# Kernel tuning notes

Hardware: AMD Instinct MI355X
Metric: run time of the kernel (lower is better)

Reference implementation:

```python
import math
import jax, jax.numpy as jnp
import numpy as np

NUM_EXPERTS = 8
CAPACITY_FACTOR = 1.5

def setup_inputs() -> dict:
    key = jax.random.key(0)
    ks = jax.random.split(key, 4)
    B, T, D, F, E = 4, 2048, 1024, 4096, NUM_EXPERTS
    scale = 0.02
    return {
        "x": jax.random.normal(ks[0], (B, T, D), dtype=jnp.float32),
        "router_w": jax.random.normal(ks[1], (E, D), dtype=jnp.float32) * scale,  # nn.Linear(D,E,bias=False).weight
        "w1": jax.random.normal(ks[2], (E, D, F), dtype=jnp.float32) * scale,
        "b1": jnp.zeros((E, F), dtype=jnp.float32),
        "w2": jax.random.normal(ks[3], (E, F, D), dtype=jnp.float32) * scale,
        "b2": jnp.zeros((E, D), dtype=jnp.float32),
    }

def reference(x, router_w, w1, b1, w2, b2):
    B, T, D = x.shape
    E = router_w.shape[0]
    N = B * T
    C = max(math.ceil(CAPACITY_FACTOR * N / E), 1)  # static per-expert capacity

    x_flat = x.reshape(N, D)
    logits = x_flat @ router_w.T                      # [N, E]
    probs = jax.nn.softmax(logits, axis=-1)
    chosen_e = jnp.argmax(probs, axis=-1)             # [N] int
    chosen_p = jnp.max(probs, axis=-1)                # [N]

    # First-come-first-served capacity: position of each token within its expert's queue
    onehot = jax.nn.one_hot(chosen_e, E, dtype=jnp.float32)          # [N, E]
    pos = jnp.take_along_axis(jnp.cumsum(onehot, axis=0), chosen_e[:, None], axis=1)[:, 0] - 1.0
    pos = pos.astype(jnp.int32)                                       # [N]
    kept = (pos < C)                                                  # [N] bool
    pos_c = jnp.clip(pos, 0, C - 1)

    # Scatter tokens into per-expert capacity buffers [E, C, D]; dropped tokens contribute 0
    buf = jnp.zeros((E, C, D), dtype=x.dtype).at[chosen_e, pos_c].add(
        x_flat * kept[:, None].astype(x.dtype))

    # Expert FFN: Linear -> exact GELU -> Linear (torch nn.GELU default = erf)
    h = jax.nn.gelu(jnp.einsum('ecd,edf->ecf', buf, w1) + b1[:, None, :], approximate=False)
    eo = jnp.einsum('ecf,efd->ecd', h, w2) + b2[:, None, :]           # [E, C, D]

    # Gather back and scale by router prob; dropped tokens get zeros
    y = eo[chosen_e, pos_c] * (chosen_p * kept.astype(x.dtype))[:, None]
    return y.reshape(B, T, D)
```

## Files before the change

kernel.cpp:

```cpp
#include <hip/hip_runtime.h>
#include <hip/hip_bf16.h>
#include <math.h>

typedef unsigned short u16;
typedef __attribute__((ext_vector_type(8))) short short8;
typedef __attribute__((ext_vector_type(4))) float f32x4;

#define NTOK 8192
#define DMODEL 1024
#define FDIM 4096
#define NEXP 8
#define CAP 1536

__device__ __forceinline__ u16 f2bf(float f) {
  __hip_bfloat16 b = __float2bfloat16(f);
  u16 u;
  __builtin_memcpy(&u, &b, 2);
  return u;
}

__device__ __forceinline__ float gelu_exact(float v) {
  float x = v * 0.70710678118654752f;
  float ax = fabsf(x);
  float t = __builtin_amdgcn_rcpf(1.0f + 0.3275911f * ax);
  float p =
      t * (0.254829592f +
           t * (-0.284496736f +
                t * (1.421413741f + t * (-1.453152027f + t * 1.061405429f))));
  float er = 1.0f - p * __expf(-ax * ax);
  er = copysignf(er, x);
  return 0.5f * v * (1.0f + er);
}

__device__ __forceinline__ void gload_lds16(const u16* g, u16* l) {
  __builtin_amdgcn_global_load_lds(
      (const __attribute__((address_space(1))) void*)g,
      (__attribute__((address_space(3))) void*)l, 16, 0, 0);
}

__global__ __launch_bounds__(256) void router_kernel(
    const float* __restrict__ x, const float* __restrict__ rw,
    int* __restrict__ chosen_e, float* __restrict__ chosen_p) {
  int b = blockIdx.x, tid = threadIdx.x;
  int tok = (b * 256 + tid) >> 6;
  int lane = tid & 63;
  const float4* xp = (const float4*)(x + (size_t)tok * DMODEL) + lane * 4;
  float4 x0 = xp[0], x1 = xp[1], x2 = xp[2], x3 = xp[3];
  float l[8];
#pragma unroll
  for (int e = 0; e < 8; e++) {
    const float4* wp = (const float4*)(rw + (size_t)e * DMODEL) + lane * 4;
    float4 w0 = wp[0], w1v = wp[1], w2v = wp[2], w3 = wp[3];
    float s = x0.x * w0.x + x0.y * w0.y + x0.z * w0.z + x0.w * w0.w;
    s += x1.x * w1v.x + x1.y * w1v.y + x1.z * w1v.z + x1.w * w1v.w;
    s += x2.x * w2v.x + x2.y * w2v.y + x2.z * w2v.z + x2.w * w2v.w;
    s += x3.x * w3.x + x3.y * w3.y + x3.z * w3.z + x3.w * w3.w;
    l[e] = s;
  }
#pragma unroll
  for (int off = 32; off > 0; off >>= 1) {
#pragma unroll
    for (int e = 0; e < 8; e++) l[e] += __shfl_xor(l[e], off, 64);
  }
  if (lane == 0) {
    float best = l[0];
    int am = 0;
#pragma unroll
    for (int e = 1; e < 8; e++)
      if (l[e] > best) { best = l[e]; am = e; }
    float denom = 0.f;
#pragma unroll
    for (int e = 0; e < 8; e++) denom += expf(l[e] - best);
    chosen_e[tok] = am;
    chosen_p[tok] = 1.0f / denom;
  }
}

__device__ __forceinline__ void trans256(const float* __restrict__ ip,
                                         u16* __restrict__ op, int Rin,
                                         int Cin, int r0, int c0, char* lds,
                                         int tid) {
  int w = tid >> 6, l = tid & 63;
#pragma unroll
  for (int i = 0; i < 16; i++) {
    int row = w * 16 + i;
    float4 v = *(const float4*)(ip + (size_t)(r0 + row) * Cin + c0 + l * 4);
    uint2 d;
    d.x = (unsigned)f2bf(v.x) | ((unsigned)f2bf(v.y) << 16);
    d.y = (unsigned)f2bf(v.z) | ((unsigned)f2bf(v.w) << 16);
    int ch = (l >> 1) ^ ((row >> 3) & 7);
    *(uint2*)(lds + row * 512 + ch * 16 + (l & 1) * 8) = d;
  }
  __syncthreads();
#pragma unroll
  for (int p = 0; p < 2; p++) {
    int c = ((tid >> 5) + p * 32) * 4;
    int rb = (tid & 31) * 8;
    short8 s0, s1, s2, s3;
#pragma unroll
    for (int j = 0; j < 8; j++) {
      int r = rb + j;
      int ch = (c >> 3) ^ ((r >> 3) & 7);
      uint2 d = *(const uint2*)(lds + r * 512 + ch * 16 + (c & 7) * 2);
      s0[j] = (short)(d.x & 0xffff);
      s1[j] = (short)(d.x >> 16);
      s2[j] = (short)(d.y & 0xffff);
      s3[j] = (short)(d.y >> 16);
    }
    u16* ob = op + (size_t)((r0 + rb) >> 5) * Cin * 32 +
              (size_t)(c0 + c) * 32 + ((r0 + rb) & 31);
    *(short8*)(ob) = s0;
    *(short8*)(ob + 32) = s1;
    *(short8*)(ob + 64) = s2;
    *(short8*)(ob + 96) = s3;
  }
}

__global__ __launch_bounds__(1024, 1) void wtrans_kernel(
    const float* __restrict__ w1, const float* __restrict__ w2,
    u16* __restrict__ w1t, u16* __restrict__ w2t,
    const int* __restrict__ chosen_e, int* __restrict__ tok_of_slot,
    int* __restrict__ counts, float* __restrict__ out) {
  extern __shared__ char lds[];
  int b = blockIdx.x, tid = threadIdx.x;
  if (b == 0) {
    if (tid < 512) {
      int w = tid >> 6, lane = tid & 63;
      unsigned long long ltmask =
          (lane == 63) ? ~0ull >> 1 : (1ull << lane) - 1ull;
      int cnt = 0;
      for (int c = 0; c < NTOK / 64; c++) {
        int i = c * 64 + lane;
        int e = chosen_e[i];
        unsigned long long bal = __ballot(e == w);
        if (e == w) {
          int p = cnt + __popcll(bal & ltmask);
          if (p < CAP) {
            tok_of_slot[w * CAP + p] = i;
          } else {
            float4 z = make_float4(0.f, 0.f, 0.f, 0.f);
            float* orow = out + (size_t)i * DMODEL;
            for (int d = 0; d < DMODEL; d += 4) *(float4*)(orow + d) = z;
          }
        }
        cnt += __popcll(bal);
      }
      for (int p = cnt + lane; p < CAP; p += 64) tok_of_slot[w * CAP + p] = -1;
      if (lane == 0) counts[w] = cnt < CAP ? cnt : CAP;
    }
  } else if (b < 513) {
    int idx = b - 1;
    int e = idx >> 6, rem = idx & 63;
    int r0 = (rem >> 4) * 256, c0 = (rem & 15) * 256;
    trans256(w1 + (size_t)e * DMODEL * FDIM, w1t + (size_t)e * DMODEL * FDIM,
             DMODEL, FDIM, r0, c0, lds, tid);
  } else {
    int idx = b - 513;
    int e = idx >> 6, rem = idx & 63;
    int r0 = (rem >> 2) * 256, c0 = (rem & 3) * 256;
    trans256(w2 + (size_t)e * DMODEL * FDIM, w2t + (size_t)e * DMODEL * FDIM,
             FDIM, DMODEL, r0, c0, lds, tid);
  }
}

__global__ __launch_bounds__(256) void gather_kernel(
    const float* __restrict__ x, const int* __restrict__ tok_of_slot,
    u16* __restrict__ xg) {
  int slot = blockIdx.x * 4 + (threadIdx.x >> 6);
  int lane = threadIdx.x & 63;
  int tok = tok_of_slot[slot];
  u16* dst = xg + (size_t)slot * DMODEL + lane * 16;
  if (tok < 0) {
    short8 z = {};
    *(short8*)(dst) = z;
    *(short8*)(dst + 8) = z;
    return;
  }
  const float4* sp = (const float4*)(x + (size_t)tok * DMODEL) + lane * 4;
  float4 a = sp[0], b = sp[1], c = sp[2], d = sp[3];
  short8 s0, s1;
  s0[0] = (short)f2bf(a.x); s0[1] = (short)f2bf(a.y);
  s0[2] = (short)f2bf(a.z); s0[3] = (short)f2bf(a.w);
  s0[4] = (short)f2bf(b.x); s0[5] = (short)f2bf(b.y);
  s0[6] = (short)f2bf(b.z); s0[7] = (short)f2bf(b.w);
  s1[0] = (short)f2bf(c.x); s1[1] = (short)f2bf(c.y);
  s1[2] = (short)f2bf(c.z); s1[3] = (short)f2bf(c.w);
  s1[4] = (short)f2bf(d.x); s1[5] = (short)f2bf(d.y);
  s1[6] = (short)f2bf(d.z); s1[7] = (short)f2bf(d.w);
  *(short8*)(dst) = s0;
  *(short8*)(dst + 8) = s1;
}

template <int NX, int NY>
__device__ __forceinline__ void tile_coords(int& bx, int& by, int& bz) {
  int flat = blockIdx.x + NX * (blockIdx.y + NY * blockIdx.z);
  int nwg = NX * NY * (int)gridDim.z;
  int swz = (flat & 7) * (nwg >> 3) + (flat >> 3);
  bx = swz % NX;
  int rem = swz / NX;
  by = rem % NY;
  bz = rem / NY;
}

template <int KD>
__device__ __forceinline__ void mainloop_db(const u16* pa0, const u16* pa1,
                                            const u16* pb0, const u16* pb1,
                                            size_t bstep, u16* smem,
                                            f32x4 (&acc)[4][4], int tid) {
  int wid = tid >> 6, lane = tid & 63;
  int wm = (wid >> 1) * 64, wn = (wid & 1) * 64;
  int fr = lane & 15, fk = (lane >> 4) * 8;
  int aro = (wm + fr) * 32 + fk;
  int bro = 4096 + (wn + fr) * 32 + fk;
  gload_lds16(pa0, smem + tid * 8);
  gload_lds16(pa1, smem + 2048 + tid * 8);
  gload_lds16(pb0, smem + 4096 + tid * 8);
  gload_lds16(pb1, smem + 6144 + tid * 8);
  __syncthreads();
  int cur = 0;
#pragma unroll 1
  for (int t = 0; t < KD / 32; ++t) {
    const u16* cb = smem + cur * 8192;
    u16* nb = smem + (cur ^ 1) * 8192;
    if (t + 1 < KD / 32) {
      gload_lds16(pa0 + (t + 1) * 32, nb + tid * 8);
      gload_lds16(pa1 + (t + 1) * 32, nb + 2048 + tid * 8);
      gload_lds16(pb0 + (size_t)(t + 1) * bstep, nb + 4096 + tid * 8);
      gload_lds16(pb1 + (size_t)(t + 1) * bstep, nb + 6144 + tid * 8);
    }
    short8 av[4], bv[4];
#pragma unroll
    for (int m = 0; m < 4; m++) av[m] = *(const short8*)(cb + aro + m * 512);
#pragma unroll
    for (int n = 0; n < 4; n++) bv[n] = *(const short8*)(cb + bro + n * 512);
#pragma unroll
    for (int m = 0; m < 4; m++)
#pragma unroll
      for (int n = 0; n < 4; n++)
        acc[m][n] = __builtin_amdgcn_mfma_f32_16x16x32_bf16(av[m], bv[n],
                                                            acc[m][n], 0, 0, 0);
    __syncthreads();
    cur ^= 1;
  }
}

#define VMWAIT(N) asm volatile("s_waitcnt vmcnt(" #N ")" ::: "memory")
#define LGKM0 asm volatile("s_waitcnt lgkmcnt(0)" ::: "memory")

#define G1_STAGE_A(t)                                              \
  {                                                                \
    u16* d_ = smem + ((t) & 3) * 16384 + tid * 8;                  \
    gload_lds16(pa0 + (t) * 32, d_);                               \
    gload_lds16(pa1 + (t) * 32, d_ + 4096);                        \
  }
#define G1_STAGE_B(t)                                              \
  {                                                                \
    u16* d_ = smem + ((t) & 3) * 16384 + 8192 + tid * 8;           \
    gload_lds16(pb0 + (size_t)(t) * (FDIM * 32), d_);              \
    gload_lds16(pb1 + (size_t)(t) * (FDIM * 32), d_ + 4096);       \
  }

#define G1_TILE(t, VMSTMT, DO_ISSUE)                                          \
  {                                                                           \
    const u16* Ab_ = smem + ((t) & 3) * 16384;                                \
    short8 a_[8], b0_, b1_;                                                   \
    _Pragma("unroll") for (int m_ = 0; m_ < 8; m_++) a_[m_] =                 \
        *(const short8*)(Ab_ + aoff + m_ * 512);                              \
    b0_ = *(const short8*)(Ab_ + boff);                                       \
    b1_ = *(const short8*)(Ab_ + boff + 512);                                 \
    if (DO_ISSUE) G1_STAGE_A((t) + 3);                                        \
    __builtin_amdgcn_s_barrier();                                             \
    LGKM0;                                                                    \
    __builtin_amdgcn_s_setprio(1);                                            \
    _Pragma("unroll") for (int m_ = 0; m_ < 8; m_++) {                        \
      acc[m_][0] = __builtin_amdgcn_mfma_f32_16x16x32_bf16(a_[m_], b0_,       \
                                                           acc[m_][0], 0, 0,  \
                                                           0);                \
      acc[m_][1] = __builtin_amdgcn_mfma_f32_16x16x32_bf16(a_[m_], b1_,       \
                                                           acc[m_][1], 0, 0,  \
                                                           0);                \
    }                                                                         \
    __builtin_amdgcn_s_setprio(0);                                            \
    __builtin_amdgcn_s_barrier();                                             \
    short8 b2_ = *(const short8*)(Ab_ + boff + 1024);                         \
    short8 b3_ = *(const short8*)(Ab_ + boff + 1536);                         \
    if (DO_ISSUE) G1_STAGE_B((t) + 3);                                        \
    VMSTMT;                                                                   \
    __builtin_amdgcn_s_barrier();                                             \
    LGKM0;                                                                    \
    __builtin_amdgcn_s_setprio(1);                                            \
    _Pragma("unroll") for (int m_ = 0; m_ < 8; m_++) {                        \
      acc[m_][2] = __builtin_amdgcn_mfma_f32_16x16x32_bf16(a_[m_], b2_,       \
                                                           acc[m_][2], 0, 0,  \
                                                           0);                \
      acc[m_][3] = __builtin_amdgcn_mfma_f32_16x16x32_bf16(a_[m_], b3_,       \
                                                           acc[m_][3], 0, 0,  \
                                                           0);                \
    }                                                                         \
    __builtin_amdgcn_s_setprio(0);                                            \
    __builtin_amdgcn_s_barrier();                                             \
  }

template <int NX, int NY>
__global__ __launch_bounds__(512, 2) void gemm1_kernel(
    const u16* __restrict__ xg, const u16* __restrict__ w1tB,
    const int* __restrict__ counts, u16* __restrict__ hB,
    const float* __restrict__ b1, int e0, long long hStrideE) {
  extern __shared__ __align__(16) u16 smem[];
  int bx, by, bz;
  tile_coords<NX, NY>(bx, by, bz);
  int e = e0 + bz;
  int m0 = by * 256, n0 = bx * 256;
  if (m0 >= counts[e]) return;
  const u16* Bg = w1tB + (size_t)e * FDIM * DMODEL;
  u16* H = hB + (size_t)bz * hStrideE;
  int tid = threadIdx.x;

  int r4 = tid >> 2, c8 = (tid & 3) * 8;
  const u16* pa0 = xg + (size_t)(e * CAP + m0 + r4) * DMODEL + c8;
  const u16* pa1 = pa0 + (size_t)128 * DMODEL;
  const u16* pb0 = Bg + (size_t)(n0 + r4) * 32 + c8;
  const u16* pb1 = pb0 + 128 * 32;

  int wid = tid >> 6, lane = tid & 63;
  int wm = (wid >> 2) * 128, wn = (wid & 3) * 64;
  int fr = lane & 15, fk = (lane >> 4) * 8;
  int aoff = (wm + fr) * 32 + fk;
  int boff = 8192 + (wn + fr) * 32 + fk;
  f32x4 acc[8][4] = {};

  G1_STAGE_A(0); G1_STAGE_B(0);
  G1_STAGE_A(1); G1_STAGE_B(1);
  G1_STAGE_A(2); G1_STAGE_B(2);
  VMWAIT(8);
  __builtin_amdgcn_s_barrier();

  const int KT = DMODEL / 32;
#pragma unroll 1
  for (int t = 0; t < KT - 3; ++t) G1_TILE(t, VMWAIT(8), true);
  G1_TILE(KT - 3, VMWAIT(4), false);
  G1_TILE(KT - 2, VMWAIT(0), false);
  G1_TILE(KT - 1, (void)0, false);

  int fq = lane >> 4;
  const float* b1g = b1 + (size_t)e * FDIM + n0;
  float bias[4];
#pragma unroll
  for (int n = 0; n < 4; n++) bias[n] = b1g[wn + n * 16 + fr];
#pragma unroll
  for (int m = 0; m < 8; m++) {
#pragma unroll
    for (int n = 0; n < 4; n++) {
      int colL = wn + n * 16 + fr;
#pragma unroll
      for (int j = 0; j < 4; j++) {
        int rL = wm + m * 16 + fq * 4 + j;
        float v = gelu_exact(acc[m][n][j] + bias[n]);
        int ch = (colL >> 3) ^ ((rL >> 2) & 7);
        smem[rL * 256 + ch * 8 + (colL & 7)] = f2bf(v);
      }
    }
  }
  __syncthreads();
#pragma unroll
  for (int p = 0; p < 16; p++) {
    int idx = p * 512 + tid;
    int rr = idx >> 5, cch = idx & 31;
    int ch = cch ^ ((rr >> 2) & 7);
    short8 v = *(const short8*)(smem + rr * 256 + ch * 8);
    *(short8*)(H + (size_t)(m0 + rr) * FDIM + n0 + cch * 8) = v;
  }
}

template <int NX, int NY>
__global__ __launch_bounds__(256) void gemm2_kernel(
    const u16* __restrict__ hB, const u16* __restrict__ w2tB,
    float* __restrict__ out, const float* __restrict__ b2,
    const int* __restrict__ tok_of_slot, const int* __restrict__ counts,
    const float* __restrict__ chosen_p, int e0, long long hStrideE) {
  __shared__ __align__(16) u16 smem[16384];
  int bx, by, bz;
  tile_coords<NX, NY>(bx, by, bz);
  int e = e0 + bz;
  int m0 = by * 128, n0 = bx * 128;
  if (m0 >= counts[e]) return;
  const u16* Ag = hB + (size_t)bz * hStrideE;
  const u16* Bg = w2tB + (size_t)e * DMODEL * FDIM;
  const float* b2g = b2 + (size_t)e * DMODEL;
  int tid = threadIdx.x;
  int r2 = tid >> 2, c8 = (tid & 3) * 8;
  const u16* pa0 = Ag + (size_t)(m0 + r2) * FDIM + c8;
  const u16* pa1 = pa0 + (size_t)64 * FDIM;
  const u16* pb0 = Bg + (size_t)(n0 + r2) * 32 + c8;
  const u16* pb1 = pb0 + 64 * 32;
  f32x4 acc[4][4] = {};
  mainloop_db<FDIM>(pa0, pa1, pb0, pb1, (size_t)DMODEL * 32, smem, acc, tid);

  int wid = tid >> 6, lane = tid & 63;
  int wm = (wid >> 1) * 64, wn = (wid & 1) * 64;
  int fr = lane & 15, fq = lane >> 4;
  float bias[4];
#pragma unroll
  for (int n = 0; n < 4; n++) bias[n] = b2g[n0 + wn + n * 16 + fr];
#pragma unroll
  for (int m = 0; m < 4; m++) {
#pragma unroll
    for (int j = 0; j < 4; j++) {
      int rL = wm + m * 16 + fq * 4 + j;
      int tk = tok_of_slot[e * CAP + m0 + rL];
      if (tk >= 0) {
        float sc = chosen_p[tk];
#pragma unroll
        for (int n = 0; n < 4; n++) {
          int colL = wn + n * 16 + fr;
          out[(size_t)tk * DMODEL + n0 + colL] = (acc[m][n][j] + bias[n]) * sc;
        }
      }
    }
  }
}

extern "C" void kernel_launch(void* const* d_in, const int* in_sizes, int n_in,
                              void* d_out, int out_size, void* d_ws,
                              size_t ws_size, hipStream_t stream) {
  const float* x = (const float*)d_in[0];
  const float* rw = (const float*)d_in[1];
  const float* w1 = (const float*)d_in[2];
  const float* b1 = (const float*)d_in[3];
  const float* w2 = (const float*)d_in[4];
  const float* b2 = (const float*)d_in[5];
  float* out = (float*)d_out;

  char* ws = (char*)d_ws;
  size_t off = 0;
  auto alloc = [&](size_t bytes) -> void* {
    void* p = ws + off;
    off = (off + bytes + 255) & ~(size_t)255;
    return p;
  };
  int* chosen_e = (int*)alloc((size_t)NTOK * 4);
  float* chosen_p = (float*)alloc((size_t)NTOK * 4);
  int* tok_of_slot = (int*)alloc((size_t)NEXP * CAP * 4);
  int* counts = (int*)alloc(NEXP * 4);
  u16* xg = (u16*)alloc((size_t)NEXP * CAP * DMODEL * 2);
  u16* w1t = (u16*)alloc((size_t)NEXP * DMODEL * FDIM * 2);
  u16* w2t = (u16*)alloc((size_t)NEXP * DMODEL * FDIM * 2);
  size_t hFull = (size_t)NEXP * CAP * FDIM * 2;
  size_t hLoop = (size_t)CAP * FDIM * 2;
  bool full = (off + hFull) <= ws_size;
  u16* h = (u16*)alloc(full ? hFull : hLoop);

  static_assert(CAP % 256 == 0 && FDIM % 256 == 0 && DMODEL % 128 == 0, "");
  const int TLDS = 131072, G1LDS = 131072;
  hipFuncSetAttribute((const void*)wtrans_kernel,
                      hipFuncAttributeMaxDynamicSharedMemorySize, TLDS);
  hipFuncSetAttribute((const void*)gemm1_kernel<FDIM / 256, CAP / 256>,
                      hipFuncAttributeMaxDynamicSharedMemorySize, G1LDS);

  router_kernel<<<NTOK / 4, 256, 0, stream>>>(x, rw, chosen_e, chosen_p);
  wtrans_kernel<<<1025, 1024, TLDS, stream>>>(w1, w2, w1t, w2t, chosen_e,
                                              tok_of_slot, counts, out);
  gather_kernel<<<NEXP * CAP / 4, 256, 0, stream>>>(x, tok_of_slot, xg);

  if (full) {
    gemm1_kernel<FDIM / 256, CAP / 256>
        <<<dim3(FDIM / 256, CAP / 256, NEXP), 512, G1LDS, stream>>>(
            xg, w1t, counts, h, b1, 0, (long long)CAP * FDIM);
    gemm2_kernel<DMODEL / 128, CAP / 128>
        <<<dim3(DMODEL / 128, CAP / 128, NEXP), 256, 0, stream>>>(
            h, w2t, out, b2, tok_of_slot, counts, chosen_p, 0,
            (long long)CAP * FDIM);
  } else {
    for (int e = 0; e < NEXP; e++) {
      gemm1_kernel<FDIM / 256, CAP / 256>
          <<<dim3(FDIM / 256, CAP / 256, 1), 512, G1LDS, stream>>>(
              xg, w1t, counts, h, b1, e, 0);
      gemm2_kernel<DMODEL / 128, CAP / 128>
          <<<dim3(DMODEL / 128, CAP / 128, 1), 256, 0, stream>>>(
              h, w2t, out, b2, tok_of_slot, counts, chosen_p, e, 0);
    }
  }
  (void)in_sizes;
  (void)n_in;
  (void)ws_size;
}
```

Before: 354.6 us.

## Load B operands directly into registers and stage only A through LDS

```diff
diff --git a/kernel.cpp b/kernel.cpp
--- a/kernel.cpp
+++ b/kernel.cpp
@@ -202,105 +202,6 @@
   bz = rem / NY;
 }
 
-template <int KD>
-__device__ __forceinline__ void mainloop_db(const u16* pa0, const u16* pa1,
-                                            const u16* pb0, const u16* pb1,
-                                            size_t bstep, u16* smem,
-                                            f32x4 (&acc)[4][4], int tid) {
-  int wid = tid >> 6, lane = tid & 63;
-  int wm = (wid >> 1) * 64, wn = (wid & 1) * 64;
-  int fr = lane & 15, fk = (lane >> 4) * 8;
-  int aro = (wm + fr) * 32 + fk;
-  int bro = 4096 + (wn + fr) * 32 + fk;
-  gload_lds16(pa0, smem + tid * 8);
-  gload_lds16(pa1, smem + 2048 + tid * 8);
-  gload_lds16(pb0, smem + 4096 + tid * 8);
-  gload_lds16(pb1, smem + 6144 + tid * 8);
-  __syncthreads();
-  int cur = 0;
-#pragma unroll 1
-  for (int t = 0; t < KD / 32; ++t) {
-    const u16* cb = smem + cur * 8192;
-    u16* nb = smem + (cur ^ 1) * 8192;
-    if (t + 1 < KD / 32) {
-      gload_lds16(pa0 + (t + 1) * 32, nb + tid * 8);
-      gload_lds16(pa1 + (t + 1) * 32, nb + 2048 + tid * 8);
-      gload_lds16(pb0 + (size_t)(t + 1) * bstep, nb + 4096 + tid * 8);
-      gload_lds16(pb1 + (size_t)(t + 1) * bstep, nb + 6144 + tid * 8);
-    }
-    short8 av[4], bv[4];
-#pragma unroll
-    for (int m = 0; m < 4; m++) av[m] = *(const short8*)(cb + aro + m * 512);
-#pragma unroll
-    for (int n = 0; n < 4; n++) bv[n] = *(const short8*)(cb + bro + n * 512);
-#pragma unroll
-    for (int m = 0; m < 4; m++)
-#pragma unroll
-      for (int n = 0; n < 4; n++)
-        acc[m][n] = __builtin_amdgcn_mfma_f32_16x16x32_bf16(av[m], bv[n],
-                                                            acc[m][n], 0, 0, 0);
-    __syncthreads();
-    cur ^= 1;
-  }
-}
-
-#define VMWAIT(N) asm volatile("s_waitcnt vmcnt(" #N ")" ::: "memory")
-#define LGKM0 asm volatile("s_waitcnt lgkmcnt(0)" ::: "memory")
-
-#define G1_STAGE_A(t)                                              \
-  {                                                                \
-    u16* d_ = smem + ((t) & 3) * 16384 + tid * 8;                  \
-    gload_lds16(pa0 + (t) * 32, d_);                               \
-    gload_lds16(pa1 + (t) * 32, d_ + 4096);                        \
-  }
-#define G1_STAGE_B(t)                                              \
-  {                                                                \
-    u16* d_ = smem + ((t) & 3) * 16384 + 8192 + tid * 8;           \
-    gload_lds16(pb0 + (size_t)(t) * (FDIM * 32), d_);              \
-    gload_lds16(pb1 + (size_t)(t) * (FDIM * 32), d_ + 4096);       \
-  }
-
-#define G1_TILE(t, VMSTMT, DO_ISSUE)                                          \
-  {                                                                           \
-    const u16* Ab_ = smem + ((t) & 3) * 16384;                                \
-    short8 a_[8], b0_, b1_;                                                   \
-    _Pragma("unroll") for (int m_ = 0; m_ < 8; m_++) a_[m_] =                 \
-        *(const short8*)(Ab_ + aoff + m_ * 512);                              \
-    b0_ = *(const short8*)(Ab_ + boff);                                       \
-    b1_ = *(const short8*)(Ab_ + boff + 512);                                 \
-    if (DO_ISSUE) G1_STAGE_A((t) + 3);                                        \
-    __builtin_amdgcn_s_barrier();                                             \
-    LGKM0;                                                                    \
-    __builtin_amdgcn_s_setprio(1);                                            \
-    _Pragma("unroll") for (int m_ = 0; m_ < 8; m_++) {                        \
-      acc[m_][0] = __builtin_amdgcn_mfma_f32_16x16x32_bf16(a_[m_], b0_,       \
-                                                           acc[m_][0], 0, 0,  \
-                                                           0);                \
-      acc[m_][1] = __builtin_amdgcn_mfma_f32_16x16x32_bf16(a_[m_], b1_,       \
-                                                           acc[m_][1], 0, 0,  \
-                                                           0);                \
-    }                                                                         \
-    __builtin_amdgcn_s_setprio(0);                                            \
-    __builtin_amdgcn_s_barrier();                                             \
-    short8 b2_ = *(const short8*)(Ab_ + boff + 1024);                         \
-    short8 b3_ = *(const short8*)(Ab_ + boff + 1536);                         \
-    if (DO_ISSUE) G1_STAGE_B((t) + 3);                                        \
-    VMSTMT;                                                                   \
-    __builtin_amdgcn_s_barrier();                                             \
-    LGKM0;                                                                    \
-    __builtin_amdgcn_s_setprio(1);                                            \
-    _Pragma("unroll") for (int m_ = 0; m_ < 8; m_++) {                        \
-      acc[m_][2] = __builtin_amdgcn_mfma_f32_16x16x32_bf16(a_[m_], b2_,       \
-                                                           acc[m_][2], 0, 0,  \
-                                                           0);                \
-      acc[m_][3] = __builtin_amdgcn_mfma_f32_16x16x32_bf16(a_[m_], b3_,       \
-                                                           acc[m_][3], 0, 0,  \
-                                                           0);                \
-    }                                                                         \
-    __builtin_amdgcn_s_setprio(0);                                            \
-    __builtin_amdgcn_s_barrier();                                             \
-  }
-
 template <int NX, int NY>
 __global__ __launch_bounds__(512, 2) void gemm1_kernel(
     const u16* __restrict__ xg, const u16* __restrict__ w1tB,
@@ -319,66 +220,102 @@
   int r4 = tid >> 2, c8 = (tid & 3) * 8;
   const u16* pa0 = xg + (size_t)(e * CAP + m0 + r4) * DMODEL + c8;
   const u16* pa1 = pa0 + (size_t)128 * DMODEL;
-  const u16* pb0 = Bg + (size_t)(n0 + r4) * 32 + c8;
-  const u16* pb1 = pb0 + 128 * 32;
 
   int wid = tid >> 6, lane = tid & 63;
-  int wm = (wid >> 2) * 128, wn = (wid & 3) * 64;
-  int fr = lane & 15, fk = (lane >> 4) * 8;
-  int aoff = (wm + fr) * 32 + fk;
-  int boff = 8192 + (wn + fr) * 32 + fk;
-  f32x4 acc[8][4] = {};
-
-  G1_STAGE_A(0); G1_STAGE_B(0);
-  G1_STAGE_A(1); G1_STAGE_B(1);
-  G1_STAGE_A(2); G1_STAGE_B(2);
-  VMWAIT(8);
-  __builtin_amdgcn_s_barrier();
-
-  const int KT = DMODEL / 32;
+  int wm = (wid >> 1) * 64, wn = (wid & 1) * 128;
+  int fr = lane & 15, fkb = (lane >> 4) * 8;
+  int aoff = (wm + fr) * 32 + fkb;
+  const u16* Bcol = Bg + (size_t)(n0 + wn + fr) * 32 + fkb;
+
+  f32x4 acc[4][8] = {};
+  short8 bA[8], bB[8];
+
+  auto stageA = [&](int t, int buf) {
+    u16* d = smem + buf * 8192 + tid * 8;
+    gload_lds16(pa0 + t * 32, d);
+    gload_lds16(pa1 + t * 32, d + 4096);
+  };
+  auto loadB = [&](short8(&bd)[8], int t) {
+    const u16* p = Bcol + (size_t)t * (FDIM * 32);
+#pragma unroll
+    for (int n = 0; n < 8; n++) bd[n] = *(const short8*)(p + n * 512);
+  };
+  auto compute = [&](int buf, short8(&bd)[8]) {
+    const u16* cb = smem + buf * 8192;
+    short8 av[4];
+#pragma unroll
+    for (int m = 0; m < 4; m++) av[m] = *(const short8*)(cb + aoff + m * 512);
+#pragma unroll
+    for (int m = 0; m < 4; m++)
+#pragma unroll
+      for (int n = 0; n < 8; n++)
+        acc[m][n] = __builtin_amdgcn_mfma_f32_16x16x32_bf16(av[m], bd[n],
+                                                            acc[m][n], 0, 0, 0);
+  };
+
+  stageA(0, 0);
+  loadB(bA, 0);
+  __syncthreads();
 #pragma unroll 1
-  for (int t = 0; t < KT - 3; ++t) G1_TILE(t, VMWAIT(8), true);
-  G1_TILE(KT - 3, VMWAIT(4), false);
-  G1_TILE(KT - 2, VMWAIT(0), false);
-  G1_TILE(KT - 1, (void)0, false);
+  for (int t = 0; t < DMODEL / 32; t += 2) {
+    if (t + 1 < DMODEL / 32) {
+      stageA(t + 1, 1);
+      loadB(bB, t + 1);
+    }
+    compute(0, bA);
+    __syncthreads();
+    if (t + 2 < DMODEL / 32) {
+      stageA(t + 2, 0);
+      loadB(bA, t + 2);
+    }
+    compute(1, bB);
+    __syncthreads();
+  }
 
   int fq = lane >> 4;
   const float* b1g = b1 + (size_t)e * FDIM + n0;
-  float bias[4];
-#pragma unroll
-  for (int n = 0; n < 4; n++) bias[n] = b1g[wn + n * 16 + fr];
-#pragma unroll
-  for (int m = 0; m < 8; m++) {
-#pragma unroll
-    for (int n = 0; n < 4; n++) {
-      int colL = wn + n * 16 + fr;
-#pragma unroll
-      for (int j = 0; j < 4; j++) {
-        int rL = wm + m * 16 + fq * 4 + j;
-        float v = gelu_exact(acc[m][n][j] + bias[n]);
-        int ch = (colL >> 3) ^ ((rL >> 2) & 7);
-        smem[rL * 256 + ch * 8 + (colL & 7)] = f2bf(v);
+  float bias[8];
+#pragma unroll
+  for (int n = 0; n < 8; n++) bias[n] = b1g[wn + n * 16 + fr];
+#pragma unroll
+  for (int half = 0; half < 2; half++) {
+    if ((wid >> 2) == half) {
+      int rbase = wm & 127;
+#pragma unroll
+      for (int m = 0; m < 4; m++) {
+#pragma unroll
+        for (int n = 0; n < 8; n++) {
+          int colL = wn + n * 16 + fr;
+#pragma unroll
+          for (int j = 0; j < 4; j++) {
+            int rL = rbase + m * 16 + fq * 4 + j;
+            float v = gelu_exact(acc[m][n][j] + bias[n]);
+            int ch = (colL >> 3) ^ ((rL >> 2) & 7);
+            smem[rL * 256 + ch * 8 + (colL & 7)] = f2bf(v);
+          }
+        }
       }
     }
-  }
-  __syncthreads();
-#pragma unroll
-  for (int p = 0; p < 16; p++) {
-    int idx = p * 512 + tid;
-    int rr = idx >> 5, cch = idx & 31;
-    int ch = cch ^ ((rr >> 2) & 7);
-    short8 v = *(const short8*)(smem + rr * 256 + ch * 8);
-    *(short8*)(H + (size_t)(m0 + rr) * FDIM + n0 + cch * 8) = v;
+    __syncthreads();
+#pragma unroll
+    for (int p = 0; p < 8; p++) {
+      int idx = p * 512 + tid;
+      int rr = idx >> 5, cch = idx & 31;
+      int ch = cch ^ ((rr >> 2) & 7);
+      short8 v = *(const short8*)(smem + rr * 256 + ch * 8);
+      *(short8*)(H + (size_t)(m0 + half * 128 + rr) * FDIM + n0 + cch * 8) = v;
+    }
+    __syncthreads();
   }
 }
 
 template <int NX, int NY>
-__global__ __launch_bounds__(256) void gemm2_kernel(
+__global__ __launch_bounds__(256, 2) void gemm2_kernel(
     const u16* __restrict__ hB, const u16* __restrict__ w2tB,
     float* __restrict__ out, const float* __restrict__ b2,
     const int* __restrict__ tok_of_slot, const int* __restrict__ counts,
     const float* __restrict__ chosen_p, int e0, long long hStrideE) {
-  __shared__ __align__(16) u16 smem[16384];
+  __shared__ __align__(16) u16 smem[8192];
   int bx, by, bz;
   tile_coords<NX, NY>(bx, by, bz);
   int e = e0 + bz;
@@ -388,17 +325,63 @@
   const u16* Bg = w2tB + (size_t)e * DMODEL * FDIM;
   const float* b2g = b2 + (size_t)e * DMODEL;
   int tid = threadIdx.x;
-  int r2 = tid >> 2, c8 = (tid & 3) * 8;
-  const u16* pa0 = Ag + (size_t)(m0 + r2) * FDIM + c8;
+
+  int r4 = tid >> 2, c8 = (tid & 3) * 8;
+  const u16* pa0 = Ag + (size_t)(m0 + r4) * FDIM + c8;
   const u16* pa1 = pa0 + (size_t)64 * FDIM;
-  const u16* pb0 = Bg + (size_t)(n0 + r2) * 32 + c8;
-  const u16* pb1 = pb0 + 64 * 32;
-  f32x4 acc[4][4] = {};
-  mainloop_db<FDIM>(pa0, pa1, pb0, pb1, (size_t)DMODEL * 32, smem, acc, tid);
 
   int wid = tid >> 6, lane = tid & 63;
   int wm = (wid >> 1) * 64, wn = (wid & 1) * 64;
-  int fr = lane & 15, fq = lane >> 4;
+  int fr = lane & 15, fkb = (lane >> 4) * 8;
+  int aoff = (wm + fr) * 32 + fkb;
+  const u16* Bcol = Bg + (size_t)(n0 + wn + fr) * 32 + fkb;
+
+  f32x4 acc[4][4] = {};
+  short8 bA[4], bB[4];
+
+  auto stageA = [&](int t, int buf) {
+    u16* d = smem + buf * 4096 + tid * 8;
+    gload_lds16(pa0 + t * 32, d);
+    gload_lds16(pa1 + t * 32, d + 2048);
+  };
+  auto loadB = [&](short8(&bd)[4], int t) {
+    const u16* p = Bcol + (size_t)t * (DMODEL * 32);
+#pragma unroll
+    for (int n = 0; n < 4; n++) bd[n] = *(const short8*)(p + n * 512);
+  };
+  auto compute = [&](int buf, short8(&bd)[4]) {
+    const u16* cb = smem + buf * 4096;
+    short8 av[4];
+#pragma unroll
+    for (int m = 0; m < 4; m++) av[m] = *(const short8*)(cb + aoff + m * 512);
+#pragma unroll
+    for (int m = 0; m < 4; m++)
+#pragma unroll
+      for (int n = 0; n < 4; n++)
+        acc[m][n] = __builtin_amdgcn_mfma_f32_16x16x32_bf16(av[m], bd[n],
+                                                            acc[m][n], 0, 0, 0);
+  };
+
+  stageA(0, 0);
+  loadB(bA, 0);
+  __syncthreads();
+#pragma unroll 1
+  for (int t = 0; t < FDIM / 32; t += 2) {
+    if (t + 1 < FDIM / 32) {
+      stageA(t + 1, 1);
+      loadB(bB, t + 1);
+    }
+    compute(0, bA);
+    __syncthreads();
+    if (t + 2 < FDIM / 32) {
+      stageA(t + 2, 0);
+      loadB(bA, t + 2);
+    }
+    compute(1, bB);
+    __syncthreads();
+  }
+
+  int fq = lane >> 4;
   float bias[4];
 #pragma unroll
   for (int n = 0; n < 4; n++) bias[n] = b2g[n0 + wn + n * 16 + fr];
@@ -451,7 +434,7 @@
   u16* h = (u16*)alloc(full ? hFull : hLoop);
 
   static_assert(CAP % 256 == 0 && FDIM % 256 == 0 && DMODEL % 128 == 0, "");
-  const int TLDS = 131072, G1LDS = 131072;
+  const int TLDS = 131072, G1LDS = 65536;
   hipFuncSetAttribute((const void*)wtrans_kernel,
                       hipFuncAttributeMaxDynamicSharedMemorySize, TLDS);
   hipFuncSetAttribute((const void*)gemm1_kernel<FDIM / 256, CAP / 256>,
```

Measured after the change: 429.2 us. 1.21x slower.

## Restructure both expert GEMM mainloops to double-buffered 64-wide K steps

Applied to the files above, without the earlier changes.

```diff
diff --git a/kernel.cpp b/kernel.cpp
--- a/kernel.cpp
+++ b/kernel.cpp
@@ -37,6 +37,11 @@
       (const __attribute__((address_space(1))) void*)g,
       (__attribute__((address_space(3))) void*)l, 16, 0, 0);
 }
+
+#define VMWAIT(N) asm volatile("s_waitcnt vmcnt(" #N ")" ::: "memory")
+#define LGKM0 asm volatile("s_waitcnt lgkmcnt(0)" ::: "memory")
+#define SB0 __builtin_amdgcn_sched_barrier(0)
+#define BAR __builtin_amdgcn_s_barrier()
 
 __global__ __launch_bounds__(256) void router_kernel(
     const float* __restrict__ x, const float* __restrict__ rw,
@@ -202,103 +207,61 @@
   bz = rem / NY;
 }
 
-template <int KD>
-__device__ __forceinline__ void mainloop_db(const u16* pa0, const u16* pa1,
-                                            const u16* pb0, const u16* pb1,
-                                            size_t bstep, u16* smem,
-                                            f32x4 (&acc)[4][4], int tid) {
-  int wid = tid >> 6, lane = tid & 63;
-  int wm = (wid >> 1) * 64, wn = (wid & 1) * 64;
-  int fr = lane & 15, fk = (lane >> 4) * 8;
-  int aro = (wm + fr) * 32 + fk;
-  int bro = 4096 + (wn + fr) * 32 + fk;
-  gload_lds16(pa0, smem + tid * 8);
-  gload_lds16(pa1, smem + 2048 + tid * 8);
-  gload_lds16(pb0, smem + 4096 + tid * 8);
-  gload_lds16(pb1, smem + 6144 + tid * 8);
-  __syncthreads();
-  int cur = 0;
-#pragma unroll 1
-  for (int t = 0; t < KD / 32; ++t) {
-    const u16* cb = smem + cur * 8192;
-    u16* nb = smem + (cur ^ 1) * 8192;
-    if (t + 1 < KD / 32) {
-      gload_lds16(pa0 + (t + 1) * 32, nb + tid * 8);
-      gload_lds16(pa1 + (t + 1) * 32, nb + 2048 + tid * 8);
-      gload_lds16(pb0 + (size_t)(t + 1) * bstep, nb + 4096 + tid * 8);
-      gload_lds16(pb1 + (size_t)(t + 1) * bstep, nb + 6144 + tid * 8);
-    }
-    short8 av[4], bv[4];
-#pragma unroll
-    for (int m = 0; m < 4; m++) av[m] = *(const short8*)(cb + aro + m * 512);
-#pragma unroll
-    for (int n = 0; n < 4; n++) bv[n] = *(const short8*)(cb + bro + n * 512);
-#pragma unroll
-    for (int m = 0; m < 4; m++)
-#pragma unroll
-      for (int n = 0; n < 4; n++)
-        acc[m][n] = __builtin_amdgcn_mfma_f32_16x16x32_bf16(av[m], bv[n],
-                                                            acc[m][n], 0, 0, 0);
-    __syncthreads();
-    cur ^= 1;
-  }
-}
-
-#define VMWAIT(N) asm volatile("s_waitcnt vmcnt(" #N ")" ::: "memory")
-#define LGKM0 asm volatile("s_waitcnt lgkmcnt(0)" ::: "memory")
-
-#define G1_STAGE_A(t)                                              \
-  {                                                                \
-    u16* d_ = smem + ((t) & 3) * 16384 + tid * 8;                  \
-    gload_lds16(pa0 + (t) * 32, d_);                               \
-    gload_lds16(pa1 + (t) * 32, d_ + 4096);                        \
-  }
-#define G1_STAGE_B(t)                                              \
-  {                                                                \
-    u16* d_ = smem + ((t) & 3) * 16384 + 8192 + tid * 8;           \
-    gload_lds16(pb0 + (size_t)(t) * (FDIM * 32), d_);              \
-    gload_lds16(pb1 + (size_t)(t) * (FDIM * 32), d_ + 4096);       \
-  }
-
-#define G1_TILE(t, VMSTMT, DO_ISSUE)                                          \
-  {                                                                           \
-    const u16* Ab_ = smem + ((t) & 3) * 16384;                                \
-    short8 a_[8], b0_, b1_;                                                   \
-    _Pragma("unroll") for (int m_ = 0; m_ < 8; m_++) a_[m_] =                 \
-        *(const short8*)(Ab_ + aoff + m_ * 512);                              \
-    b0_ = *(const short8*)(Ab_ + boff);                                       \
-    b1_ = *(const short8*)(Ab_ + boff + 512);                                 \
-    if (DO_ISSUE) G1_STAGE_A((t) + 3);                                        \
-    __builtin_amdgcn_s_barrier();                                             \
-    LGKM0;                                                                    \
-    __builtin_amdgcn_s_setprio(1);                                            \
-    _Pragma("unroll") for (int m_ = 0; m_ < 8; m_++) {                        \
-      acc[m_][0] = __builtin_amdgcn_mfma_f32_16x16x32_bf16(a_[m_], b0_,       \
-                                                           acc[m_][0], 0, 0,  \
-                                                           0);                \
-      acc[m_][1] = __builtin_amdgcn_mfma_f32_16x16x32_bf16(a_[m_], b1_,       \
-                                                           acc[m_][1], 0, 0,  \
-                                                           0);                \
-    }                                                                         \
-    __builtin_amdgcn_s_setprio(0);                                            \
-    __builtin_amdgcn_s_barrier();                                             \
-    short8 b2_ = *(const short8*)(Ab_ + boff + 1024);                         \
-    short8 b3_ = *(const short8*)(Ab_ + boff + 1536);                         \
-    if (DO_ISSUE) G1_STAGE_B((t) + 3);                                        \
-    VMSTMT;                                                                   \
-    __builtin_amdgcn_s_barrier();                                             \
-    LGKM0;                                                                    \
-    __builtin_amdgcn_s_setprio(1);                                            \
-    _Pragma("unroll") for (int m_ = 0; m_ < 8; m_++) {                        \
-      acc[m_][2] = __builtin_amdgcn_mfma_f32_16x16x32_bf16(a_[m_], b2_,       \
-                                                           acc[m_][2], 0, 0,  \
-                                                           0);                \
-      acc[m_][3] = __builtin_amdgcn_mfma_f32_16x16x32_bf16(a_[m_], b3_,       \
-                                                           acc[m_][3], 0, 0,  \
-                                                           0);                \
-    }                                                                         \
-    __builtin_amdgcn_s_setprio(0);                                            \
-    __builtin_amdgcn_s_barrier();                                             \
+#define G1_STAGE_A(t, kk)                                           \
+  {                                                                 \
+    u16* d_ = smem + ((t)&1) * 32768 + (kk)*8192 + tid * 8;         \
+    const u16* s_ = paA + (size_t)(t)*64 + (kk)*32;                 \
+    gload_lds16(s_, d_);                                            \
+    gload_lds16(s_ + (size_t)128 * DMODEL, d_ + 4096);              \
+  }
+#define G1_STAGE_B(t, kk)                                           \
+  {                                                                 \
+    u16* d_ = smem + ((t)&1) * 32768 + 16384 + (kk)*8192 + tid * 8; \
+    const u16* s_ = paB + (size_t)(2 * (t) + (kk)) * (FDIM * 32);   \
+    gload_lds16(s_, d_);                                            \
+    gload_lds16(s_ + 4096, d_ + 4096);                              \
+  }
+#define G1_LDA(kk)                                                  \
+  _Pragma("unroll") for (int m_ = 0; m_ < 8; m_++) a_[m_] =         \
+      *(const short8*)(smem + bufo + (kk)*8192 + aoff + m_ * 512);
+#define G1_LDB(kk, n, dst)                                          \
+  dst = *(const short8*)(smem + bufo + 16384 + (kk)*8192 + boff + (n)*512);
+#define G1_MFMA(B0, B1, c0, c1)                                             \
+  __builtin_amdgcn_s_setprio(1);                                            \
+  _Pragma("unroll") for (int m_ = 0; m_ < 8; m_++) {                        \
+    acc[m_][c0] = __builtin_amdgcn_mfma_f32_16x16x32_bf16(a_[m_], B0,       \
+                                                          acc[m_][c0], 0,   \
+                                                          0, 0);            \
+    acc[m_][c1] = __builtin_amdgcn_mfma_f32_16x16x32_bf16(a_[m_], B1,       \
+                                                          acc[m_][c1], 0,   \
+                                                          0, 0);            \
+  }                                                                         \
+  __builtin_amdgcn_s_setprio(0);
+
+#define G1_STEP(t, DO_STAGE, W2, W4)                                \
+  {                                                                 \
+    const int bufo = ((t)&1) * 32768;                               \
+    short8 a_[8], b0_, b1_;                                         \
+    G1_LDA(0); G1_LDB(0, 0, b0_); G1_LDB(0, 1, b1_);                \
+    if (DO_STAGE) G1_STAGE_A((t) + 1, 0);                           \
+    BAR; LGKM0; SB0;                                                \
+    G1_MFMA(b0_, b1_, 0, 1);                                        \
+    BAR;                                                            \
+    G1_LDB(0, 2, b0_); G1_LDB(0, 3, b1_);                           \
+    if (DO_STAGE) G1_STAGE_B((t) + 1, 0);                           \
+    BAR; LGKM0; SB0;                                                \
+    G1_MFMA(b0_, b1_, 2, 3);                                        \
+    W2; BAR;                                                        \
+    G1_LDA(1); G1_LDB(1, 0, b0_); G1_LDB(1, 1, b1_);                \
+    if (DO_STAGE) G1_STAGE_A((t) + 1, 1);                           \
+    BAR; LGKM0; SB0;                                                \
+    G1_MFMA(b0_, b1_, 0, 1);                                        \
+    BAR;                                                            \
+    G1_LDB(1, 2, b0_); G1_LDB(1, 3, b1_);                           \
+    if (DO_STAGE) G1_STAGE_B((t) + 1, 1);                           \
+    BAR; LGKM0; SB0;                                                \
+    G1_MFMA(b0_, b1_, 2, 3);                                        \
+    W4; BAR;                                                        \
   }
 
 template <int NX, int NY>
@@ -316,31 +279,28 @@
   u16* H = hB + (size_t)bz * hStrideE;
   int tid = threadIdx.x;
 
-  int r4 = tid >> 2, c8 = (tid & 3) * 8;
-  const u16* pa0 = xg + (size_t)(e * CAP + m0 + r4) * DMODEL + c8;
-  const u16* pa1 = pa0 + (size_t)128 * DMODEL;
-  const u16* pb0 = Bg + (size_t)(n0 + r4) * 32 + c8;
-  const u16* pb1 = pb0 + 128 * 32;
+  const u16* paA = xg + (size_t)(e * CAP + m0 + (tid >> 2)) * DMODEL +
+                   (tid & 3) * 8;
+  const u16* paB = Bg + (size_t)n0 * 32 + tid * 8;
 
   int wid = tid >> 6, lane = tid & 63;
   int wm = (wid >> 2) * 128, wn = (wid & 3) * 64;
   int fr = lane & 15, fk = (lane >> 4) * 8;
   int aoff = (wm + fr) * 32 + fk;
-  int boff = 8192 + (wn + fr) * 32 + fk;
+  int boff = (wn + fr) * 32 + fk;
   f32x4 acc[8][4] = {};
 
-  G1_STAGE_A(0); G1_STAGE_B(0);
-  G1_STAGE_A(1); G1_STAGE_B(1);
-  G1_STAGE_A(2); G1_STAGE_B(2);
-  VMWAIT(8);
-  __builtin_amdgcn_s_barrier();
-
-  const int KT = DMODEL / 32;
+  G1_STAGE_A(0, 0);
+  G1_STAGE_B(0, 0);
+  G1_STAGE_A(0, 1);
+  G1_STAGE_B(0, 1);
+  VMWAIT(4);
+  BAR;
+
+  const int KT = DMODEL / 64;
 #pragma unroll 1
-  for (int t = 0; t < KT - 3; ++t) G1_TILE(t, VMWAIT(8), true);
-  G1_TILE(KT - 3, VMWAIT(4), false);
-  G1_TILE(KT - 2, VMWAIT(0), false);
-  G1_TILE(KT - 1, (void)0, false);
+  for (int t = 0; t < KT - 1; ++t) G1_STEP(t, true, VMWAIT(4), VMWAIT(4));
+  G1_STEP(KT - 1, false, VMWAIT(0), (void)0);
 
   int fq = lane >> 4;
   const float* b1g = b1 + (size_t)e * FDIM + n0;
@@ -372,13 +332,70 @@
   }
 }
 
+#define G2_STAGE_A(t, kk)                                           \
+  {                                                                 \
+    u16* d_ = smem + ((t)&1) * 16384 + (kk)*4096 + tid * 8;         \
+    const u16* s_ = paA + (size_t)(t)*64 + (kk)*32;                 \
+    gload_lds16(s_, d_);                                            \
+    gload_lds16(s_ + (size_t)64 * FDIM, d_ + 2048);                 \
+  }
+#define G2_STAGE_B(t, kk)                                           \
+  {                                                                 \
+    u16* d_ = smem + ((t)&1) * 16384 + 8192 + (kk)*4096 + tid * 8;  \
+    const u16* s_ = paB + (size_t)(2 * (t) + (kk)) * (DMODEL * 32); \
+    gload_lds16(s_, d_);                                            \
+    gload_lds16(s_ + 2048, d_ + 2048);                              \
+  }
+#define G2_LDA(kk)                                                  \
+  _Pragma("unroll") for (int m_ = 0; m_ < 4; m_++) a_[m_] =         \
+      *(const short8*)(smem + bufo + (kk)*4096 + aoff + m_ * 512);
+#define G2_LDB(kk, n, dst)                                          \
+  dst = *(const short8*)(smem + bufo + 8192 + (kk)*4096 + boff + (n)*512);
+#define G2_MFMA(B0, B1, c0, c1)                                             \
+  __builtin_amdgcn_s_setprio(1);                                            \
+  _Pragma("unroll") for (int m_ = 0; m_ < 4; m_++) {                        \
+    acc[m_][c0] = __builtin_amdgcn_mfma_f32_16x16x32_bf16(a_[m_], B0,       \
+                                                          acc[m_][c0], 0,   \
+                                                          0, 0);            \
+    acc[m_][c1] = __builtin_amdgcn_mfma_f32_16x16x32_bf16(a_[m_], B1,       \
+                                                          acc[m_][c1], 0,   \
+                                                          0, 0);            \
+  }                                                                         \
+  __builtin_amdgcn_s_setprio(0);
+
+#define G2_STEP(t, DO_STAGE, W2, W4)                                \
+  {                                                                 \
+    const int bufo = ((t)&1) * 16384;                               \
+    short8 a_[4], b0_, b1_;                                         \
+    G2_LDA(0); G2_LDB(0, 0, b0_); G2_LDB(0, 1, b1_);                \
+    if (DO_STAGE) G2_STAGE_A((t) + 1, 0);                           \
+    BAR; LGKM0; SB0;                                                \
+    G2_MFMA(b0_, b1_, 0, 1);                                        \
+    BAR;                                                            \
+    G2_LDB(0, 2, b0_); G2_LDB(0, 3, b1_);                           \
+    if (DO_STAGE) G2_STAGE_B((t) + 1, 0);                           \
+    BAR; LGKM0; SB0;                                                \
+    G2_MFMA(b0_, b1_, 2, 3);                                        \
+    W2; BAR;                                                        \
+    G2_LDA(1); G2_LDB(1, 0, b0_); G2_LDB(1, 1, b1_);                \
+    if (DO_STAGE) G2_STAGE_A((t) + 1, 1);                           \
+    BAR; LGKM0; SB0;                                                \
+    G2_MFMA(b0_, b1_, 0, 1);                                        \
+    BAR;                                                            \
+    G2_LDB(1, 2, b0_); G2_LDB(1, 3, b1_);                           \
+    if (DO_STAGE) G2_STAGE_B((t) + 1, 1);                           \
+    BAR; LGKM0; SB0;                                                \
+    G2_MFMA(b0_, b1_, 2, 3);                                        \
+    W4; BAR;                                                        \
+  }
+
 template <int NX, int NY>
-__global__ __launch_bounds__(256) void gemm2_kernel(
+__global__ __launch_bounds__(256, 2) void gemm2_kernel(
     const u16* __restrict__ hB, const u16* __restrict__ w2tB,
     float* __restrict__ out, const float* __restrict__ b2,
     const int* __restrict__ tok_of_slot, const int* __restrict__ counts,
     const float* __restrict__ chosen_p, int e0, long long hStrideE) {
-  __shared__ __align__(16) u16 smem[16384];
+  extern __shared__ __align__(16) u16 smem[];
   int bx, by, bz;
   tile_coords<NX, NY>(bx, by, bz);
   int e = e0 + bz;
@@ -388,17 +405,30 @@
   const u16* Bg = w2tB + (size_t)e * DMODEL * FDIM;
   const float* b2g = b2 + (size_t)e * DMODEL;
   int tid = threadIdx.x;
-  int r2 = tid >> 2, c8 = (tid & 3) * 8;
-  const u16* pa0 = Ag + (size_t)(m0 + r2) * FDIM + c8;
-  const u16* pa1 = pa0 + (size_t)64 * FDIM;
-  const u16* pb0 = Bg + (size_t)(n0 + r2) * 32 + c8;
-  const u16* pb1 = pb0 + 64 * 32;
-  f32x4 acc[4][4] = {};
-  mainloop_db<FDIM>(pa0, pa1, pb0, pb1, (size_t)DMODEL * 32, smem, acc, tid);
+
+  const u16* paA = Ag + (size_t)(m0 + (tid >> 2)) * FDIM + (tid & 3) * 8;
+  const u16* paB = Bg + (size_t)n0 * 32 + tid * 8;
 
   int wid = tid >> 6, lane = tid & 63;
   int wm = (wid >> 1) * 64, wn = (wid & 1) * 64;
-  int fr = lane & 15, fq = lane >> 4;
+  int fr = lane & 15, fk = (lane >> 4) * 8;
+  int aoff = (wm + fr) * 32 + fk;
+  int boff = (wn + fr) * 32 + fk;
+  f32x4 acc[4][4] = {};
+
+  G2_STAGE_A(0, 0);
+  G2_STAGE_B(0, 0);
+  G2_STAGE_A(0, 1);
+  G2_STAGE_B(0, 1);
+  VMWAIT(4);
+  BAR;
+
+  const int KT = FDIM / 64;
+#pragma unroll 1
+  for (int t = 0; t < KT - 1; ++t) G2_STEP(t, true, VMWAIT(4), VMWAIT(4));
+  G2_STEP(KT - 1, false, VMWAIT(0), (void)0);
+
+  int fq = lane >> 4;
   float bias[4];
 #pragma unroll
   for (int n = 0; n < 4; n++) bias[n] = b2g[n0 + wn + n * 16 + fr];
@@ -451,11 +481,13 @@
   u16* h = (u16*)alloc(full ? hFull : hLoop);
 
   static_assert(CAP % 256 == 0 && FDIM % 256 == 0 && DMODEL % 128 == 0, "");
-  const int TLDS = 131072, G1LDS = 131072;
+  const int TLDS = 131072, G1LDS = 131072, G2LDS = 65536;
   hipFuncSetAttribute((const void*)wtrans_kernel,
                       hipFuncAttributeMaxDynamicSharedMemorySize, TLDS);
   hipFuncSetAttribute((const void*)gemm1_kernel<FDIM / 256, CAP / 256>,
                       hipFuncAttributeMaxDynamicSharedMemorySize, G1LDS);
+  hipFuncSetAttribute((const void*)gemm2_kernel<DMODEL / 128, CAP / 128>,
+                      hipFuncAttributeMaxDynamicSharedMemorySize, G2LDS);
 
   router_kernel<<<NTOK / 4, 256, 0, stream>>>(x, rw, chosen_e, chosen_p);
   wtrans_kernel<<<1025, 1024, TLDS, stream>>>(w1, w2, w1t, w2t, chosen_e,
@@ -467,7 +499,7 @@
         <<<dim3(FDIM / 256, CAP / 256, NEXP), 512, G1LDS, stream>>>(
             xg, w1t, counts, h, b1, 0, (long long)CAP * FDIM);
     gemm2_kernel<DMODEL / 128, CAP / 128>
-        <<<dim3(DMODEL / 128, CAP / 128, NEXP), 256, 0, stream>>>(
+        <<<dim3(DMODEL / 128, CAP / 128, NEXP), 256, G2LDS, stream>>>(
             h, w2t, out, b2, tok_of_slot, counts, chosen_p, 0,
             (long long)CAP * FDIM);
   } else {
@@ -476,7 +508,7 @@
           <<<dim3(FDIM / 256, CAP / 256, 1), 512, G1LDS, stream>>>(
               xg, w1t, counts, h, b1, e, 0);
       gemm2_kernel<DMODEL / 128, CAP / 128>
-          <<<dim3(DMODEL / 128, CAP / 128, 1), 256, 0, stream>>>(
+          <<<dim3(DMODEL / 128, CAP / 128, 1), 256, G2LDS, stream>>>(
               h, w2t, out, b2, tok_of_slot, counts, chosen_p, e, 0);
     }
   }
```

Result: slower. 375.6 us (+5.9%).
